# Kernel tuning notes

Hardware: AMD Instinct MI355X
Metric: run time of the kernel (lower is better)

## Reference

```python
import jax, jax.numpy as jnp
import numpy as np

L = 3
EPSILON = 0.01
T = 1.0
L1_EPS = 1e-12  # torch F.normalize default eps


def _cdist(x, y):
    # Euclidean pairwise distance, (b, n, d) x (b, m, d) -> (b, n, m)
    x2 = jnp.sum(x * x, axis=-1, keepdims=True)            # (b, n, 1)
    y2 = jnp.sum(y * y, axis=-1)[:, None, :]               # (b, 1, m)
    xy = jnp.einsum('bnd,bmd->bnm', x, y)                  # (b, n, m)
    return jnp.sqrt(jnp.maximum(x2 + y2 - 2.0 * xy, 0.0))


def setup_inputs() -> dict:
    key = jax.random.key(0)
    k1, k2 = jax.random.split(key)
    B, S, D = 4, 2048, 512
    A = jax.random.uniform(k1, (B, S, S), dtype=jnp.float32)
    V = jax.random.normal(k2, (B, S, D), dtype=jnp.float32)
    return {"A": A, "V": V}


def reference(A, V):
    M = jnp.matmul(A, V)  # (b, s, d)
    for _ in range(L):
        Md = jax.lax.stop_gradient(M)
        Vd = jax.lax.stop_gradient(V)
        dist = _cdist(Md, Vd)                               # (b, s, s)
        w = 1.0 / (dist + EPSILON)                          # norm == 'L2'
        ww = w * A                                          # (b, s, s)
        l1 = jnp.maximum(jnp.sum(jnp.abs(ww), axis=-1, keepdims=True), L1_EPS)
        ww_norm = ww / l1
        M = (1.0 - T) * M + T * jnp.matmul(ww_norm, V)
    return M
```

## Files before the change

### kernel.cpp

```cpp
#include <hip/hip_runtime.h>


typedef __bf16 bf16;
typedef bf16 bf16x4 __attribute__((ext_vector_type(4)));
typedef bf16 bf16x8 __attribute__((ext_vector_type(8)));
typedef float f32x4 __attribute__((ext_vector_type(4)));

#define S_DIM 2048
#define D_DIM 512
#define NB    4
#define EPSILON 0.01f

__global__ void cast_kernel(const float* __restrict__ in, bf16* __restrict__ out, int n4) {
  int i = blockIdx.x * blockDim.x + threadIdx.x;
  if (i >= n4) return;
  float4 v = ((const float4*)in)[i];
  bf16x4 o = { (bf16)v.x, (bf16)v.y, (bf16)v.z, (bf16)v.w };
  ((bf16x4*)out)[i] = o;
}

__global__ void vprep_kernel(const float* __restrict__ V, bf16* __restrict__ Vbf,
                             bf16* __restrict__ Vt, float* __restrict__ v2) {
  __shared__ float tile[64][68];
  int b  = blockIdx.y;
  int r0 = blockIdx.x * 64;
  const float* Vb = V   + (size_t)b * S_DIM * D_DIM;
  bf16*       Vfb = Vbf + (size_t)b * S_DIM * D_DIM;
  bf16*       Vtb = Vt  + (size_t)b * S_DIM * D_DIM;
  float*      v2b = v2  + (size_t)b * S_DIM;
  int tx = threadIdx.x & 15, ty = threadIdx.x >> 4;
  float acc2[4] = { 0.f, 0.f, 0.f, 0.f };
  for (int c = 0; c < 8; ++c) {
    int c0 = c * 64;
#pragma unroll
    for (int i = 0; i < 4; ++i) {
      int r = ty + i * 16;
      float4 v = *(const float4*)(Vb + (size_t)(r0 + r) * D_DIM + (c0 + tx * 4));
      tile[r][tx * 4 + 0] = v.x; tile[r][tx * 4 + 1] = v.y;
      tile[r][tx * 4 + 2] = v.z; tile[r][tx * 4 + 3] = v.w;
      bf16x4 o = { (bf16)v.x, (bf16)v.y, (bf16)v.z, (bf16)v.w };
      *(bf16x4*)(Vfb + (size_t)(r0 + r) * D_DIM + (c0 + tx * 4)) = o;
#pragma unroll
      for (int j = 0; j < 4; ++j) { float f = (float)o[j]; acc2[i] += f * f; }
    }
    __syncthreads();
#pragma unroll
    for (int i = 0; i < 4; ++i) {
      int cc = ty + i * 16;
      bf16x4 o = { (bf16)tile[tx * 4 + 0][cc], (bf16)tile[tx * 4 + 1][cc],
                   (bf16)tile[tx * 4 + 2][cc], (bf16)tile[tx * 4 + 3][cc] };
      *(bf16x4*)(Vtb + (size_t)(c0 + cc) * S_DIM + (r0 + tx * 4)) = o;
    }
    __syncthreads();
  }
#pragma unroll
  for (int i = 0; i < 4; ++i) {
    float s = acc2[i];
    s += __shfl_xor(s, 1); s += __shfl_xor(s, 2);
    s += __shfl_xor(s, 4); s += __shfl_xor(s, 8);
    if (tx == 0) v2b[r0 + ty + i * 16] = s;
  }
}

template <int MODE>
__global__ __launch_bounds__(256, 4)
void gemm_kernel(const bf16* __restrict__ Amat, const bf16* __restrict__ Bmat,
                 int M, int N, int K,
                 bf16* __restrict__ Cp,
                 const float* __restrict__ m2, const float* __restrict__ v2,
                 const bf16* __restrict__ Aw, bf16* __restrict__ Wout,
                 float* __restrict__ l1p) {
  int bz, ks, kbeg, kend;
  if (MODE == 4) { bz = blockIdx.z >> 1; ks = blockIdx.z & 1; kbeg = ks * (K >> 1); kend = kbeg + (K >> 1); }
  else           { bz = blockIdx.z;      ks = 0;              kbeg = 0;             kend = K; }

  const int gx  = gridDim.x;
  const int nwg = gx * gridDim.y;
  int lin = blockIdx.y * gx + blockIdx.x;
  lin = (lin & 7) * (nwg >> 3) + (lin >> 3);
  const int bx = lin % gx;
  const int by = lin / gx;

  const int row0 = by * 128;
  const int col0 = bx * 128;
  const bf16* Ab = Amat + (size_t)bz * M * K;
  const bf16* Bb = Bmat + (size_t)bz * N * K;

  __shared__ char smem[33792];
  bf16*  ldsA = (bf16*)smem;
  bf16*  ldsB = (bf16*)(smem + 16384);
  float* ldsW = (float*)smem;

  const int tid  = threadIdx.x;
  const int wave = tid >> 6;
  const int lane = tid & 63;
  const int wr   = wave >> 1;
  const int wc   = wave & 1;
  const int q    = lane >> 4;
  const int c16  = lane & 15;

  const int srow = lane >> 3;
  const int scol = ((lane & 7) ^ srow) * 8;

  f32x4 acc[4][4] = {};

  for (int k0 = kbeg; k0 < kend; k0 += 64) {
#pragma unroll
    for (int i = 0; i < 4; ++i) {
      int slot = wave * 4 + i;
      int r = slot * 8 + srow;
      __builtin_amdgcn_global_load_lds(
          (const __attribute__((address_space(1))) void*)(Ab + (size_t)(row0 + r) * K + (k0 + scol)),
          (__attribute__((address_space(3))) void*)(ldsA + slot * 512), 16, 0, 0);
      __builtin_amdgcn_global_load_lds(
          (const __attribute__((address_space(1))) void*)(Bb + (size_t)(col0 + r) * K + (k0 + scol)),
          (__attribute__((address_space(3))) void*)(ldsB + slot * 512), 16, 0, 0);
    }
    __syncthreads();

#pragma unroll
    for (int kk = 0; kk < 2; ++kk) {
      bf16x8 afr[4], bfr[4];
#pragma unroll
      for (int mt = 0; mt < 4; ++mt) {
        int R = wr * 64 + mt * 16 + c16;
        int p = ((kk << 2) + q) ^ (c16 & 7);
        afr[mt] = *(const bf16x8*)(ldsA + (size_t)R * 64 + p * 8);
      }
#pragma unroll
      for (int nt = 0; nt < 4; ++nt) {
        int R = wc * 64 + nt * 16 + c16;
        int p = ((kk << 2) + q) ^ (c16 & 7);
        bfr[nt] = *(const bf16x8*)(ldsB + (size_t)R * 64 + p * 8);
      }
#pragma unroll
      for (int mt = 0; mt < 4; ++mt)
#pragma unroll
        for (int nt = 0; nt < 4; ++nt)
          acc[mt][nt] = __builtin_amdgcn_mfma_f32_16x16x32_bf16(afr[mt], bfr[nt], acc[mt][nt], 0, 0, 0);
    }
    __syncthreads();
  }

  const int rowBase = row0 + wr * 64 + q * 4;
  const int colBase = col0 + wc * 64 + c16;

  if (MODE == 1) {
    const float* m2b = m2 + (size_t)bz * M;
    const float* v2b = v2 + (size_t)bz * N;
    float v2v[4];
#pragma unroll
    for (int nt = 0; nt < 4; ++nt) v2v[nt] = v2b[colBase + nt * 16];
#pragma unroll
    for (int mt = 0; mt < 4; ++mt)
#pragma unroll
      for (int r = 0; r < 4; ++r) {
        float m2v = m2b[rowBase + mt * 16 + r];
#pragma unroll
        for (int nt = 0; nt < 4; ++nt) {
          float d2 = fmaxf(m2v + v2v[nt] - 2.f * acc[mt][nt][r], 0.f);
          acc[mt][nt][r] = __builtin_amdgcn_rcpf(__builtin_amdgcn_sqrtf(d2) + EPSILON);
        }
      }
  }

  const int lr  = tid >> 3;
  const int sub = tid & 7;
#pragma unroll
  for (int h = 0; h < 2; ++h) {
    __syncthreads();
    if (wr == h) {
#pragma unroll
      for (int mt = 0; mt < 4; ++mt)
#pragma unroll
        for (int nt = 0; nt < 4; ++nt)
#pragma unroll
          for (int r = 0; r < 4; ++r)
            ldsW[(mt * 16 + q * 4 + r) * 132 + wc * 64 + nt * 16 + c16] = acc[mt][nt][r];
    }
    __syncthreads();
#pragma unroll
    for (int h2 = 0; h2 < 2; ++h2) {
      int rloc = lr + 32 * h2;
      int gi = row0 + 64 * h + rloc;
      const float* wp = ldsW + rloc * 132 + sub * 16;
      float4 w0 = *(const float4*)(wp + 0);
      float4 w1 = *(const float4*)(wp + 4);
      float4 w2 = *(const float4*)(wp + 8);
      float4 w3 = *(const float4*)(wp + 12);
      float wv_[16] = { w0.x, w0.y, w0.z, w0.w, w1.x, w1.y, w1.z, w1.w,
                        w2.x, w2.y, w2.z, w2.w, w3.x, w3.y, w3.z, w3.w };
      if (MODE == 1) {
        const bf16* ap = Aw + (size_t)bz * M * N + (size_t)gi * N + (col0 + sub * 16);
        bf16x8 a0 = *(const bf16x8*)(ap);
        bf16x8 a1 = *(const bf16x8*)(ap + 8);
        bf16x8 o0, o1;
        float rs = 0.f;
#pragma unroll
        for (int e = 0; e < 8; ++e) {
          float x0 = wv_[e] * (float)a0[e];
          float x1 = wv_[e + 8] * (float)a1[e];
          o0[e] = (bf16)x0; o1[e] = (bf16)x1;
          rs += fabsf(x0) + fabsf(x1);
        }
        bf16* op = Wout + (size_t)bz * M * N + (size_t)gi * N + (col0 + sub * 16);
        *(bf16x8*)(op)     = o0;
        *(bf16x8*)(op + 8) = o1;
        rs += __shfl_xor(rs, 1);
        rs += __shfl_xor(rs, 2);
        rs += __shfl_xor(rs, 4);
        if (sub == 0) l1p[((size_t)bx * NB + bz) * M + gi] = rs;
      } else {
        bf16* Cb = Cp + ((size_t)ks * NB + bz) * ((size_t)M * N);
        bf16x8 o0, o1;
#pragma unroll
        for (int e = 0; e < 8; ++e) { o0[e] = (bf16)wv_[e]; o1[e] = (bf16)wv_[e + 8]; }
        bf16* op = Cb + (size_t)gi * N + (col0 + sub * 16);
        *(bf16x8*)(op)     = o0;
        *(bf16x8*)(op + 8) = o1;
      }
    }
  }
}

template <int RMODE>
__global__ void reduce_kernel(const bf16* __restrict__ part, const float* __restrict__ l1p,
                              bf16* __restrict__ Mo, float* __restrict__ Fo,
                              float* __restrict__ m2) {
  int wave = threadIdx.x >> 6, lane = threadIdx.x & 63;
  int rg = blockIdx.x * 4 + wave;
  const bf16* p0 = part + (size_t)rg * D_DIM + lane * 8;
  const bf16* p1 = p0 + (size_t)NB * S_DIM * D_DIM;
  bf16x8 a = *(const bf16x8*)p0;
  bf16x8 b = *(const bf16x8*)p1;
  float v[8];
#pragma unroll
  for (int e = 0; e < 8; ++e) v[e] = (float)a[e] + (float)b[e];
  float sc = 1.f;
  if (RMODE >= 1) {
    int bb = rg >> 11, row = rg & (S_DIM - 1);
    float l1v = 0.f;
#pragma unroll
    for (int e = 0; e < 16; ++e) l1v += l1p[((size_t)e * NB + bb) * S_DIM + row];
    sc = __builtin_amdgcn_rcpf(fmaxf(l1v, 1e-12f));
  }
  float s = 0.f;
#pragma unroll
  for (int e = 0; e < 8; ++e) { v[e] *= sc; s += v[e] * v[e]; }
  if (RMODE == 2) {
    float4 o0 = { v[0], v[1], v[2], v[3] }, o1 = { v[4], v[5], v[6], v[7] };
    float* op = Fo + (size_t)rg * D_DIM + lane * 8;
    *(float4*)(op) = o0; *(float4*)(op + 4) = o1;
  } else {
    bf16x8 o;
#pragma unroll
    for (int e = 0; e < 8; ++e) o[e] = (bf16)v[e];
    *(bf16x8*)(Mo + (size_t)rg * D_DIM + lane * 8) = o;
#pragma unroll
    for (int off = 32; off > 0; off >>= 1) s += __shfl_xor(s, off);
    if (lane == 0) m2[rg] = s;
  }
}

extern "C" void kernel_launch(void* const* d_in, const int* in_sizes, int n_in,
                              void* d_out, int out_size, void* d_ws, size_t ws_size,
                              hipStream_t stream) {
  const float* A = (const float*)d_in[0];
  const float* V = (const float*)d_in[1];
  float* out = (float*)d_out;

  char* ws = (char*)d_ws;
  bf16* Abf = (bf16*)ws;   ws += (size_t)NB * S_DIM * S_DIM * 2;
  bf16* Vbf = (bf16*)ws;   ws += (size_t)NB * S_DIM * D_DIM * 2;
  bf16* Vt  = (bf16*)ws;   ws += (size_t)NB * S_DIM * D_DIM * 2;
  bf16* Mbf = (bf16*)ws;   ws += (size_t)NB * S_DIM * D_DIM * 2;
  bf16* Wbf = (bf16*)ws;   ws += (size_t)NB * S_DIM * S_DIM * 2;
  bf16* part = (bf16*)ws;  ws += (size_t)2 * NB * S_DIM * D_DIM * 2;
  float* v2 = (float*)ws;  ws += (size_t)NB * S_DIM * 4;
  float* m2 = (float*)ws;  ws += (size_t)NB * S_DIM * 4;
  float* l1p = (float*)ws; ws += (size_t)16 * NB * S_DIM * 4;

  int nA4 = NB * S_DIM * S_DIM / 4;
  cast_kernel<<<nA4 / 256, 256, 0, stream>>>(A, Abf, nA4);
  vprep_kernel<<<dim3(S_DIM / 64, NB), 256, 0, stream>>>(V, Vbf, Vt, v2);

  gemm_kernel<4><<<dim3(D_DIM / 128, S_DIM / 128, NB * 2), 256, 0, stream>>>(
      Abf, Vt, S_DIM, D_DIM, S_DIM, part, nullptr, nullptr, nullptr, nullptr, nullptr);
  reduce_kernel<0><<<NB * S_DIM / 4, 256, 0, stream>>>(part, nullptr, Mbf, nullptr, m2);

  for (int it = 0; it < 3; ++it) {
    gemm_kernel<1><<<dim3(S_DIM / 128, S_DIM / 128, NB), 256, 0, stream>>>(
        Mbf, Vbf, S_DIM, S_DIM, D_DIM, nullptr, m2, v2, Abf, Wbf, l1p);
    gemm_kernel<4><<<dim3(D_DIM / 128, S_DIM / 128, NB * 2), 256, 0, stream>>>(
        Wbf, Vt, S_DIM, D_DIM, S_DIM, part, nullptr, nullptr, nullptr, nullptr, nullptr);
    if (it < 2)
      reduce_kernel<1><<<NB * S_DIM / 4, 256, 0, stream>>>(part, l1p, Mbf, nullptr, m2);
    else
      reduce_kernel<2><<<NB * S_DIM / 4, 256, 0, stream>>>(part, l1p, nullptr, out, nullptr);
  }
}
```

Before: 321.3 us.

## Replace split-K GEMM plus reduce with full-K 128x64 GEMM and fused epilogue

```diff
diff --git a/kernel.cpp b/kernel.cpp
--- a/kernel.cpp
+++ b/kernel.cpp
@@ -11,7 +11,12 @@
 #define NB    4
 #define EPSILON 0.01f
 
-__global__ void cast_kernel(const float* __restrict__ in, bf16* __restrict__ out, int n4) {
+#define AS1 __attribute__((address_space(1)))
+#define AS3 __attribute__((address_space(3)))
+
+__global__ void cast_kernel(const float* __restrict__ in, bf16* __restrict__ out,
+                            int n4, float* __restrict__ m2z) {
+  if (blockIdx.x < 32) m2z[blockIdx.x * 256 + threadIdx.x] = 0.f;
   int i = blockIdx.x * blockDim.x + threadIdx.x;
   if (i >= n4) return;
   float4 v = ((const float4*)in)[i];
@@ -62,24 +67,22 @@
   }
 }
 
-template <int MODE>
 __global__ __launch_bounds__(256, 4)
-void gemm_kernel(const bf16* __restrict__ Amat, const bf16* __restrict__ Bmat,
-                 int M, int N, int K,
-                 bf16* __restrict__ Cp,
-                 const float* __restrict__ m2, const float* __restrict__ v2,
-                 const bf16* __restrict__ Aw, bf16* __restrict__ Wout,
-                 float* __restrict__ l1p) {
-  int bz, ks, kbeg, kend;
-  if (MODE == 4) { bz = blockIdx.z >> 1; ks = blockIdx.z & 1; kbeg = ks * (K >> 1); kend = kbeg + (K >> 1); }
-  else           { bz = blockIdx.z;      ks = 0;              kbeg = 0;             kend = K; }
-
+void gemmP_kernel(const bf16* __restrict__ Amat, const bf16* __restrict__ Bmat,
+                  int M, int N, int K,
+                  const float* __restrict__ m2, const float* __restrict__ v2,
+                  const bf16* __restrict__ Aw, bf16* __restrict__ Wout,
+                  float* __restrict__ l1p, float* __restrict__ m2z) {
+  const int bz = blockIdx.z;
   const int gx  = gridDim.x;
   const int nwg = gx * gridDim.y;
   int lin = blockIdx.y * gx + blockIdx.x;
   lin = (lin & 7) * (nwg >> 3) + (lin >> 3);
   const int bx = lin % gx;
   const int by = lin / gx;
+
+  if (bx == 0 && threadIdx.x < 128)
+    m2z[(size_t)bz * S_DIM + by * 128 + threadIdx.x] = 0.f;
 
   const int row0 = by * 128;
   const int col0 = bx * 128;
@@ -98,23 +101,22 @@
   const int wc   = wave & 1;
   const int q    = lane >> 4;
   const int c16  = lane & 15;
-
   const int srow = lane >> 3;
   const int scol = ((lane & 7) ^ srow) * 8;
 
   f32x4 acc[4][4] = {};
 
-  for (int k0 = kbeg; k0 < kend; k0 += 64) {
+  for (int k0 = 0; k0 < K; k0 += 64) {
 #pragma unroll
     for (int i = 0; i < 4; ++i) {
       int slot = wave * 4 + i;
       int r = slot * 8 + srow;
       __builtin_amdgcn_global_load_lds(
-          (const __attribute__((address_space(1))) void*)(Ab + (size_t)(row0 + r) * K + (k0 + scol)),
-          (__attribute__((address_space(3))) void*)(ldsA + slot * 512), 16, 0, 0);
+          (const AS1 void*)(Ab + (size_t)(row0 + r) * K + (k0 + scol)),
+          (AS3 void*)(ldsA + slot * 512), 16, 0, 0);
       __builtin_amdgcn_global_load_lds(
-          (const __attribute__((address_space(1))) void*)(Bb + (size_t)(col0 + r) * K + (k0 + scol)),
-          (__attribute__((address_space(3))) void*)(ldsB + slot * 512), 16, 0, 0);
+          (const AS1 void*)(Bb + (size_t)(col0 + r) * K + (k0 + scol)),
+          (AS3 void*)(ldsB + slot * 512), 16, 0, 0);
     }
     __syncthreads();
 
@@ -145,7 +147,7 @@
   const int rowBase = row0 + wr * 64 + q * 4;
   const int colBase = col0 + wc * 64 + c16;
 
-  if (MODE == 1) {
+  {
     const float* m2b = m2 + (size_t)bz * M;
     const float* v2b = v2 + (size_t)bz * N;
     float v2v[4];
@@ -190,75 +192,157 @@
       float4 w3 = *(const float4*)(wp + 12);
       float wv_[16] = { w0.x, w0.y, w0.z, w0.w, w1.x, w1.y, w1.z, w1.w,
                         w2.x, w2.y, w2.z, w2.w, w3.x, w3.y, w3.z, w3.w };
-      if (MODE == 1) {
-        const bf16* ap = Aw + (size_t)bz * M * N + (size_t)gi * N + (col0 + sub * 16);
-        bf16x8 a0 = *(const bf16x8*)(ap);
-        bf16x8 a1 = *(const bf16x8*)(ap + 8);
-        bf16x8 o0, o1;
-        float rs = 0.f;
-#pragma unroll
-        for (int e = 0; e < 8; ++e) {
-          float x0 = wv_[e] * (float)a0[e];
-          float x1 = wv_[e + 8] * (float)a1[e];
-          o0[e] = (bf16)x0; o1[e] = (bf16)x1;
-          rs += fabsf(x0) + fabsf(x1);
-        }
-        bf16* op = Wout + (size_t)bz * M * N + (size_t)gi * N + (col0 + sub * 16);
-        *(bf16x8*)(op)     = o0;
-        *(bf16x8*)(op + 8) = o1;
-        rs += __shfl_xor(rs, 1);
-        rs += __shfl_xor(rs, 2);
-        rs += __shfl_xor(rs, 4);
-        if (sub == 0) l1p[((size_t)bx * NB + bz) * M + gi] = rs;
-      } else {
-        bf16* Cb = Cp + ((size_t)ks * NB + bz) * ((size_t)M * N);
-        bf16x8 o0, o1;
-#pragma unroll
-        for (int e = 0; e < 8; ++e) { o0[e] = (bf16)wv_[e]; o1[e] = (bf16)wv_[e + 8]; }
-        bf16* op = Cb + (size_t)gi * N + (col0 + sub * 16);
-        *(bf16x8*)(op)     = o0;
-        *(bf16x8*)(op + 8) = o1;
-      }
-    }
-  }
-}
-
-template <int RMODE>
-__global__ void reduce_kernel(const bf16* __restrict__ part, const float* __restrict__ l1p,
-                              bf16* __restrict__ Mo, float* __restrict__ Fo,
-                              float* __restrict__ m2) {
-  int wave = threadIdx.x >> 6, lane = threadIdx.x & 63;
-  int rg = blockIdx.x * 4 + wave;
-  const bf16* p0 = part + (size_t)rg * D_DIM + lane * 8;
-  const bf16* p1 = p0 + (size_t)NB * S_DIM * D_DIM;
-  bf16x8 a = *(const bf16x8*)p0;
-  bf16x8 b = *(const bf16x8*)p1;
-  float v[8];
-#pragma unroll
-  for (int e = 0; e < 8; ++e) v[e] = (float)a[e] + (float)b[e];
-  float sc = 1.f;
-  if (RMODE >= 1) {
-    int bb = rg >> 11, row = rg & (S_DIM - 1);
-    float l1v = 0.f;
-#pragma unroll
-    for (int e = 0; e < 16; ++e) l1v += l1p[((size_t)e * NB + bb) * S_DIM + row];
-    sc = __builtin_amdgcn_rcpf(fmaxf(l1v, 1e-12f));
-  }
-  float s = 0.f;
-#pragma unroll
-  for (int e = 0; e < 8; ++e) { v[e] *= sc; s += v[e] * v[e]; }
-  if (RMODE == 2) {
-    float4 o0 = { v[0], v[1], v[2], v[3] }, o1 = { v[4], v[5], v[6], v[7] };
-    float* op = Fo + (size_t)rg * D_DIM + lane * 8;
-    *(float4*)(op) = o0; *(float4*)(op + 4) = o1;
-  } else {
-    bf16x8 o;
-#pragma unroll
-    for (int e = 0; e < 8; ++e) o[e] = (bf16)v[e];
-    *(bf16x8*)(Mo + (size_t)rg * D_DIM + lane * 8) = o;
-#pragma unroll
-    for (int off = 32; off > 0; off >>= 1) s += __shfl_xor(s, off);
-    if (lane == 0) m2[rg] = s;
+      const bf16* ap = Aw + (size_t)bz * M * N + (size_t)gi * N + (col0 + sub * 16);
+      bf16x8 a0 = *(const bf16x8*)(ap);
+      bf16x8 a1 = *(const bf16x8*)(ap + 8);
+      bf16x8 o0, o1;
+      float rs = 0.f;
+#pragma unroll
+      for (int e = 0; e < 8; ++e) {
+        float x0 = wv_[e] * (float)a0[e];
+        float x1 = wv_[e + 8] * (float)a1[e];
+        o0[e] = (bf16)x0; o1[e] = (bf16)x1;
+        rs += fabsf(x0) + fabsf(x1);
+      }
+      bf16* op = Wout + (size_t)bz * M * N + (size_t)gi * N + (col0 + sub * 16);
+      *(bf16x8*)(op)     = o0;
+      *(bf16x8*)(op + 8) = o1;
+      rs += __shfl_xor(rs, 1);
+      rs += __shfl_xor(rs, 2);
+      rs += __shfl_xor(rs, 4);
+      if (sub == 0) l1p[((size_t)bx * NB + bz) * M + gi] = rs;
+    }
+  }
+}
+
+template <int SCALED>
+__global__ __launch_bounds__(256, 4)
+void gemmwv_kernel(const bf16* __restrict__ Amat, const bf16* __restrict__ Bmat,
+                   const float* __restrict__ l1p, bf16* __restrict__ Mo,
+                   float* __restrict__ Fo, float* __restrict__ m2out) {
+  const int bz = blockIdx.z;
+  const int gx  = gridDim.x;
+  const int nwg = gx * gridDim.y;
+  int lin = blockIdx.y * gx + blockIdx.x;
+  lin = (lin & 7) * (nwg >> 3) + (lin >> 3);
+  const int bx = lin % gx;
+  const int by = lin / gx;
+
+  const int row0 = by * 128;
+  const int col0 = bx * 64;
+  const bf16* Ab = Amat + (size_t)bz * S_DIM * S_DIM;
+  const bf16* Bb = Bmat + (size_t)bz * S_DIM * D_DIM;
+
+  __shared__ char smem[24576];
+  bf16*  ldsA = (bf16*)smem;
+  bf16*  ldsB = (bf16*)(smem + 16384);
+  float* ldsW = (float*)smem;
+
+  const int tid  = threadIdx.x;
+  const int wave = tid >> 6;
+  const int lane = tid & 63;
+  const int wr   = wave >> 1;
+  const int wc   = wave & 1;
+  const int q    = lane >> 4;
+  const int c16  = lane & 15;
+  const int srow = lane >> 3;
+  const int scol = ((lane & 7) ^ srow) * 8;
+
+  f32x4 acc[4][2] = {};
+
+  for (int k0 = 0; k0 < S_DIM; k0 += 64) {
+#pragma unroll
+    for (int i = 0; i < 4; ++i) {
+      int slot = wave * 4 + i;
+      int r = slot * 8 + srow;
+      __builtin_amdgcn_global_load_lds(
+          (const AS1 void*)(Ab + (size_t)(row0 + r) * S_DIM + (k0 + scol)),
+          (AS3 void*)(ldsA + slot * 512), 16, 0, 0);
+    }
+#pragma unroll
+    for (int i = 0; i < 2; ++i) {
+      int slot = wave * 2 + i;
+      int r = slot * 8 + srow;
+      __builtin_amdgcn_global_load_lds(
+          (const AS1 void*)(Bb + (size_t)(col0 + r) * S_DIM + (k0 + scol)),
+          (AS3 void*)(ldsB + slot * 512), 16, 0, 0);
+    }
+    __syncthreads();
+
+#pragma unroll
+    for (int kk = 0; kk < 2; ++kk) {
+      bf16x8 afr[4], bfr[2];
+      const int p = ((kk << 2) + q) ^ (c16 & 7);
+#pragma unroll
+      for (int mt = 0; mt < 4; ++mt)
+        afr[mt] = *(const bf16x8*)(ldsA + (size_t)(wr * 64 + mt * 16 + c16) * 64 + p * 8);
+#pragma unroll
+      for (int nt = 0; nt < 2; ++nt)
+        bfr[nt] = *(const bf16x8*)(ldsB + (size_t)(wc * 32 + nt * 16 + c16) * 64 + p * 8);
+#pragma unroll
+      for (int mt = 0; mt < 4; ++mt)
+#pragma unroll
+        for (int nt = 0; nt < 2; ++nt)
+          acc[mt][nt] = __builtin_amdgcn_mfma_f32_16x16x32_bf16(afr[mt], bfr[nt], acc[mt][nt], 0, 0, 0);
+    }
+    __syncthreads();
+  }
+
+  const int lr  = tid >> 2;
+  const int sub = tid & 3;
+#pragma unroll
+  for (int h = 0; h < 2; ++h) {
+    __syncthreads();
+    if (wr == h) {
+#pragma unroll
+      for (int mt = 0; mt < 4; ++mt)
+#pragma unroll
+        for (int nt = 0; nt < 2; ++nt)
+#pragma unroll
+          for (int r = 0; r < 4; ++r)
+            ldsW[(mt * 16 + q * 4 + r) * 68 + wc * 32 + nt * 16 + c16] = acc[mt][nt][r];
+    }
+    __syncthreads();
+    const int gi = row0 + 64 * h + lr;
+    const float* wp = ldsW + lr * 68 + sub * 16;
+    float4 w0 = *(const float4*)(wp + 0);
+    float4 w1 = *(const float4*)(wp + 4);
+    float4 w2 = *(const float4*)(wp + 8);
+    float4 w3 = *(const float4*)(wp + 12);
+    float wv_[16] = { w0.x, w0.y, w0.z, w0.w, w1.x, w1.y, w1.z, w1.w,
+                      w2.x, w2.y, w2.z, w2.w, w3.x, w3.y, w3.z, w3.w };
+    float sc = 1.f;
+    if (SCALED >= 1) {
+      float l1v = 0.f;
+#pragma unroll
+      for (int e = 0; e < 16; ++e) l1v += l1p[((size_t)e * NB + bz) * S_DIM + gi];
+      sc = __builtin_amdgcn_rcpf(fmaxf(l1v, 1e-12f));
+    }
+#pragma unroll
+    for (int e = 0; e < 16; ++e) wv_[e] *= sc;
+    if (SCALED == 2) {
+      float* op = Fo + (size_t)bz * S_DIM * D_DIM + (size_t)gi * D_DIM + col0 + sub * 16;
+      float4 o0 = { wv_[0], wv_[1], wv_[2], wv_[3] };
+      float4 o1 = { wv_[4], wv_[5], wv_[6], wv_[7] };
+      float4 o2 = { wv_[8], wv_[9], wv_[10], wv_[11] };
+      float4 o3 = { wv_[12], wv_[13], wv_[14], wv_[15] };
+      *(float4*)(op + 0)  = o0; *(float4*)(op + 4)  = o1;
+      *(float4*)(op + 8)  = o2; *(float4*)(op + 12) = o3;
+    } else {
+      bf16x8 o0, o1;
+      float s = 0.f;
+#pragma unroll
+      for (int e = 0; e < 8; ++e) {
+        o0[e] = (bf16)wv_[e];     s += wv_[e] * wv_[e];
+        o1[e] = (bf16)wv_[e + 8]; s += wv_[e + 8] * wv_[e + 8];
+      }
+      bf16* op = Mo + (size_t)bz * S_DIM * D_DIM + (size_t)gi * D_DIM + col0 + sub * 16;
+      *(bf16x8*)(op)     = o0;
+      *(bf16x8*)(op + 8) = o1;
+      s += __shfl_xor(s, 1);
+      s += __shfl_xor(s, 2);
+      if (sub == 0) atomicAdd(m2out + (size_t)bz * S_DIM + gi, s);
+    }
   }
 }
 
@@ -275,27 +359,30 @@
   bf16* Vt  = (bf16*)ws;   ws += (size_t)NB * S_DIM * D_DIM * 2;
   bf16* Mbf = (bf16*)ws;   ws += (size_t)NB * S_DIM * D_DIM * 2;
   bf16* Wbf = (bf16*)ws;   ws += (size_t)NB * S_DIM * S_DIM * 2;
-  bf16* part = (bf16*)ws;  ws += (size_t)2 * NB * S_DIM * D_DIM * 2;
   float* v2 = (float*)ws;  ws += (size_t)NB * S_DIM * 4;
-  float* m2 = (float*)ws;  ws += (size_t)NB * S_DIM * 4;
+  float* m2a = (float*)ws; ws += (size_t)NB * S_DIM * 4;
+  float* m2b = (float*)ws; ws += (size_t)NB * S_DIM * 4;
   float* l1p = (float*)ws; ws += (size_t)16 * NB * S_DIM * 4;
 
   int nA4 = NB * S_DIM * S_DIM / 4;
-  cast_kernel<<<nA4 / 256, 256, 0, stream>>>(A, Abf, nA4);
+  cast_kernel<<<nA4 / 256, 256, 0, stream>>>(A, Abf, nA4, m2a);
   vprep_kernel<<<dim3(S_DIM / 64, NB), 256, 0, stream>>>(V, Vbf, Vt, v2);
 
-  gemm_kernel<4><<<dim3(D_DIM / 128, S_DIM / 128, NB * 2), 256, 0, stream>>>(
-      Abf, Vt, S_DIM, D_DIM, S_DIM, part, nullptr, nullptr, nullptr, nullptr, nullptr);
-  reduce_kernel<0><<<NB * S_DIM / 4, 256, 0, stream>>>(part, nullptr, Mbf, nullptr, m2);
-
-  for (int it = 0; it < 3; ++it) {
-    gemm_kernel<1><<<dim3(S_DIM / 128, S_DIM / 128, NB), 256, 0, stream>>>(
-        Mbf, Vbf, S_DIM, S_DIM, D_DIM, nullptr, m2, v2, Abf, Wbf, l1p);
-    gemm_kernel<4><<<dim3(D_DIM / 128, S_DIM / 128, NB * 2), 256, 0, stream>>>(
-        Wbf, Vt, S_DIM, D_DIM, S_DIM, part, nullptr, nullptr, nullptr, nullptr, nullptr);
-    if (it < 2)
-      reduce_kernel<1><<<NB * S_DIM / 4, 256, 0, stream>>>(part, l1p, Mbf, nullptr, m2);
-    else
-      reduce_kernel<2><<<NB * S_DIM / 4, 256, 0, stream>>>(part, l1p, nullptr, out, nullptr);
-  }
-}
+  gemmwv_kernel<0><<<dim3(D_DIM / 64, S_DIM / 128, NB), 256, 0, stream>>>(
+      Abf, Vt, nullptr, Mbf, nullptr, m2a);
+
+  gemmP_kernel<<<dim3(16, 16, NB), 256, 0, stream>>>(
+      Mbf, Vbf, S_DIM, S_DIM, D_DIM, m2a, v2, Abf, Wbf, l1p, m2b);
+  gemmwv_kernel<1><<<dim3(D_DIM / 64, S_DIM / 128, NB), 256, 0, stream>>>(
+      Wbf, Vt, l1p, Mbf, nullptr, m2b);
+
+  gemmP_kernel<<<dim3(16, 16, NB), 256, 0, stream>>>(
+      Mbf, Vbf, S_DIM, S_DIM, D_DIM, m2b, v2, Abf, Wbf, l1p, m2a);
+  gemmwv_kernel<1><<<dim3(D_DIM / 64, S_DIM / 128, NB), 256, 0, stream>>>(
+      Wbf, Vt, l1p, Mbf, nullptr, m2a);
+
+  gemmP_kernel<<<dim3(16, 16, NB), 256, 0, stream>>>(
+      Mbf, Vbf, S_DIM, S_DIM, D_DIM, m2a, v2, Abf, Wbf, l1p, m2b);
+  gemmwv_kernel<2><<<dim3(D_DIM / 64, S_DIM / 128, NB), 256, 0, stream>>>(
+      Wbf, Vt, l1p, nullptr, out, nullptr);
+}
```

New measurement: 328.2 us. 2.2% more time.
